# Performance work log

Measured on AMD Instinct MI355X. Metric: run time of the kernel, lower is better.

## Reference

```python
import jax, jax.numpy as jnp
import numpy as np


def setup_inputs() -> dict:
    key = jax.random.key(0)
    kq, kk, kv = jax.random.split(key, 3)
    B, H, S, D = 2, 16, 2048, 128
    q = jax.random.normal(kq, (B, H, S, D), dtype=jnp.float32)
    k = jax.random.normal(kk, (B, H, S, D), dtype=jnp.float32)
    v = jax.random.normal(kv, (B, H, S, D), dtype=jnp.float32)
    return {"q": q, "k": k, "v": v}


def reference(q, k, v):
    # qk: [B,H,S,S] full score matrix (faithful to the naive torch module)
    qk = jnp.einsum("bhsd,bhtd->bhst", q, k)
    m = jnp.max(qk, axis=-1, keepdims=True)          # row max
    p = jnp.exp(qk - m)                               # unnormalized probs
    # NOTE: original module computes lse but returns only the UNNORMALIZED o.
    o = jnp.einsum("bhst,bhtd->bhsd", p, v)
    return o
```

## Files before the change

### kernel.cpp

```cpp
#include <hip/hip_runtime.h>

typedef _Float16 f16x8  __attribute__((ext_vector_type(8)));
typedef _Float16 f16x4  __attribute__((ext_vector_type(4)));
typedef _Float16 f16x2  __attribute__((ext_vector_type(2)));
typedef float    f32x4  __attribute__((ext_vector_type(4)));
typedef float    f32x16 __attribute__((ext_vector_type(16)));
typedef int      i32x2  __attribute__((ext_vector_type(2)));

#define MFMA32(a, b, c) __builtin_amdgcn_mfma_f32_32x32x16_f16((a), (b), (c), 0, 0, 0)

static constexpr int SEQ   = 2048;
static constexpr int DIM   = 128;
static constexpr int QBLK  = 128;
static constexpr int KVBLK = 32;
static constexpr int NKT   = SEQ / KVBLK;
static constexpr int BH    = 2 * 16;
static constexpr int KSTR  = 136;
static constexpr int VSTR  = 40;

__global__ __launch_bounds__(256, 2)
void fa_fwd_kernel(const float* __restrict__ Qg, const float* __restrict__ Kg,
                   const float* __restrict__ Vg, float* __restrict__ Og)
{
    __shared__ __align__(16) _Float16 Ksh[2][KVBLK * KSTR];
    __shared__ __align__(16) _Float16 Vt[2][DIM * VSTR];

    const int tid  = threadIdx.x;
    const int wv   = tid >> 6;
    const int lane = tid & 63;
    const int lq   = lane & 31;
    const int lh   = lane >> 5;

    const int bi = blockIdx.x;
    const int bh = (bi & 7) + 8 * (bi >> 7);
    const int qt = (bi >> 3) & 15;

    const size_t base = (size_t)bh * SEQ * DIM;
    const float* Qp = Qg + base;
    const float* Kp = Kg + base;
    const float* Vp = Vg + base;
    float*       Op = Og + base;

    const int q0 = qt * QBLK + wv * 32;

    constexpr float LOG2E = 1.44269504088896340736f;
    f16x8 qh[8];
    {
        const float* qs = Qp + (size_t)(q0 + lq) * DIM + 8 * lh;
#pragma unroll
        for (int t = 0; t < 8; ++t) {
            const float4 a = *(const float4*)(qs + 16 * t);
            const float4 b = *(const float4*)(qs + 16 * t + 4);
            float xs[8] = {a.x, a.y, a.z, a.w, b.x, b.y, b.z, b.w};
            f16x8 h;
#pragma unroll
            for (int e = 0; e < 8; ++e) h[e] = (_Float16)(xs[e] * LOG2E);
            qh[t] = h;
        }
    }

    f32x16 acc[4];
#pragma unroll
    for (int a = 0; a < 4; ++a)
#pragma unroll
        for (int r = 0; r < 16; ++r) acc[a][r] = 0.0f;

    float mrow  = -3.0e38f;
    float mtrue = -3.0e38f;

    const int ksr = tid >> 3, kc0 = (tid & 7) * 16;
    const int vc  = tid & 31;
    const int vk  = (tid >> 5) * 4;
    const float* kb = Kp + (size_t)ksr * DIM + kc0;
    const float* vb = Vp + (size_t)vk * DIM + vc;

    float4 kreg[4];
    float  vreg[4][4];

    auto stage = [&](int b) {
#pragma unroll
        for (int g = 0; g < 2; ++g) {
            float xs[8] = {kreg[2*g].x, kreg[2*g].y, kreg[2*g].z, kreg[2*g].w,
                           kreg[2*g+1].x, kreg[2*g+1].y, kreg[2*g+1].z, kreg[2*g+1].w};
            f16x8 h;
#pragma unroll
            for (int e = 0; e < 8; ++e) h[e] = (_Float16)xs[e];
            *(f16x8*)((char*)&Ksh[b][0] + (ksr * KSTR + kc0 + 8 * g) * 2) = h;
        }
#pragma unroll
        for (int j = 0; j < 4; ++j) {
            const int d = vc + 32 * j;
            f16x4 tv = {(_Float16)vreg[j][0], (_Float16)vreg[j][1],
                        (_Float16)vreg[j][2], (_Float16)vreg[j][3]};
            *(f16x4*)((char*)&Vt[b][0] + (d * VSTR + vk) * 2) = tv;
        }
    };
    auto loadT = [&](int t) {
        const float* ks_ = kb + (size_t)t * KVBLK * DIM;
        const float* vs_ = vb + (size_t)t * KVBLK * DIM;
#pragma unroll
        for (int u = 0; u < 4; ++u) kreg[u] = *(const float4*)(ks_ + u * 4);
#pragma unroll
        for (int j = 0; j < 4; ++j)
#pragma unroll
            for (int r = 0; r < 4; ++r) vreg[j][r] = vs_[(size_t)r * DIM + 32 * j];
    };

    loadT(0);
    stage(0);
    loadT(1);

    for (int kt = 0; kt < NKT; ++kt) {
        const int cur = kt & 1;
        __syncthreads();

        if (kt + 1 < NKT) stage(cur ^ 1);
        if (kt + 2 < NKT) loadT(kt + 2);
        __builtin_amdgcn_sched_barrier(0);

        const char* Kc = (const char*)&Ksh[cur][0];
        const char* Vc = (const char*)&Vt[cur][0];
        f32x16 s0, s1;
#pragma unroll
        for (int r = 0; r < 16; ++r) { s0[r] = 0.0f; s1[r] = 0.0f; }
        __builtin_amdgcn_s_setprio(1);
#pragma unroll
        for (int t = 0; t < 4; ++t) {
            f16x8 ka = *(const f16x8*)(Kc + (lq * KSTR + 32 * t + 8 * lh) * 2);
            f16x8 kc = *(const f16x8*)(Kc + (lq * KSTR + 32 * t + 16 + 8 * lh) * 2);
            s0 = MFMA32(ka, qh[2 * t], s0);
            s1 = MFMA32(kc, qh[2 * t + 1], s1);
        }
        __builtin_amdgcn_s_setprio(0);
        f32x16 st = s0 + s1;

        float tmax = fmaxf(fmaxf(fmaxf(st[0], st[1]), fmaxf(st[2], st[3])),
                           fmaxf(fmaxf(st[4], st[5]), fmaxf(st[6], st[7])));
        tmax = fmaxf(tmax, fmaxf(fmaxf(fmaxf(st[8], st[9]), fmaxf(st[10], st[11])),
                                 fmaxf(fmaxf(st[12], st[13]), fmaxf(st[14], st[15]))));
        tmax = fmaxf(tmax, __shfl_xor(tmax, 32));
        mtrue = fmaxf(mtrue, tmax);

        if (!__all(tmax - mrow <= 6.0f)) {
            const float mn  = fmaxf(mrow, tmax);
            const float scl = __builtin_exp2f(mrow - mn);
            mrow = mn;
#pragma unroll
            for (int a = 0; a < 4; ++a)
#pragma unroll
                for (int r = 0; r < 16; ++r) acc[a][r] *= scl;
        }

        int pk[8];
#pragma unroll
        for (int i = 0; i < 8; ++i) {
            f16x2 e = {(_Float16)__builtin_exp2f(st[2 * i] - mrow),
                       (_Float16)__builtin_exp2f(st[2 * i + 1] - mrow)};
            pk[i] = __builtin_bit_cast(int, e);
        }

#pragma unroll
        for (int s = 0; s < 2; ++s) {
            i32x2 w02 = __builtin_amdgcn_permlane32_swap(pk[4*s+0], pk[4*s+2], false, false);
            i32x2 w13 = __builtin_amdgcn_permlane32_swap(pk[4*s+1], pk[4*s+3], false, false);
            union { int i[4]; f16x8 v; } u;
            u.i[0] = w02[0]; u.i[1] = w13[0]; u.i[2] = w02[1]; u.i[3] = w13[1];
            const f16x8 pb = u.v;
            __builtin_amdgcn_s_setprio(1);
#pragma unroll
            for (int dm = 0; dm < 4; ++dm) {
                const int d = dm * 32 + lq;
                f16x8 va = *(const f16x8*)(Vc + (d * VSTR + 16 * s + 8 * lh) * 2);
                acc[dm] = MFMA32(va, pb, acc[dm]);
            }
            __builtin_amdgcn_s_setprio(0);
        }
    }

    const float fin = __builtin_exp2f(mrow - mtrue);
#pragma unroll
    for (int a = 0; a < 4; ++a)
#pragma unroll
        for (int r = 0; r < 16; ++r) acc[a][r] *= fin;

    float* ob = Op + (size_t)(q0 + lq) * DIM + 4 * lh;
#pragma unroll
    for (int dm = 0; dm < 4; ++dm)
#pragma unroll
        for (int kp = 0; kp < 4; ++kp) {
            f32x4 v4 = {acc[dm][4*kp], acc[dm][4*kp+1], acc[dm][4*kp+2], acc[dm][4*kp+3]};
            *(f32x4*)(ob + dm * 32 + kp * 8) = v4;
        }
}

extern "C" void kernel_launch(void* const* d_in, const int* in_sizes, int n_in,
                              void* d_out, int out_size, void* d_ws, size_t ws_size,
                              hipStream_t stream) {
    const float* q = (const float*)d_in[0];
    const float* k = (const float*)d_in[1];
    const float* v = (const float*)d_in[2];
    float* o = (float*)d_out;
    dim3 grid((SEQ / QBLK) * BH);
    fa_fwd_kernel<<<grid, dim3(256), 0, stream>>>(q, k, v, o);
}
```

Before: 116.3 us.

## Double KV tile to 64 rows and speculatively compute exponentials before max update

Raises the KV tile from 32 to 64 keys, so each iteration computes two independent 32-key score blocks, halves the number of barriers, and uses wider f16x8 V-transpose stores. Exponentials are now computed with the old running max before the row max is known, and are recomputed only in the rare branch where the max grows by more than the threshold. This takes the max reduction off the critical path before the exp work. In exchange it uses more registers for the K/V prefetch and the second score block, which may hurt occupancy at 2 blocks per CU, and the LDS footprint grows.

```diff
diff --git a/kernel.cpp b/kernel.cpp
--- a/kernel.cpp
+++ b/kernel.cpp
@@ -12,11 +12,11 @@
 static constexpr int SEQ   = 2048;
 static constexpr int DIM   = 128;
 static constexpr int QBLK  = 128;
-static constexpr int KVBLK = 32;
+static constexpr int KVBLK = 64;
 static constexpr int NKT   = SEQ / KVBLK;
 static constexpr int BH    = 2 * 16;
 static constexpr int KSTR  = 136;
-static constexpr int VSTR  = 40;
+static constexpr int VSTR  = 72;
 
 __global__ __launch_bounds__(256, 2)
 void fa_fwd_kernel(const float* __restrict__ Qg, const float* __restrict__ Kg,
@@ -68,18 +68,18 @@
     float mrow  = -3.0e38f;
     float mtrue = -3.0e38f;
 
-    const int ksr = tid >> 3, kc0 = (tid & 7) * 16;
+    const int ksr = tid >> 2, kc0 = (tid & 3) * 32;
     const int vc  = tid & 31;
-    const int vk  = (tid >> 5) * 4;
+    const int vk  = (tid >> 5) * 8;
     const float* kb = Kp + (size_t)ksr * DIM + kc0;
     const float* vb = Vp + (size_t)vk * DIM + vc;
 
-    float4 kreg[4];
-    float  vreg[4][4];
+    float4 kreg[8];
+    float  vreg[4][8];
 
     auto stage = [&](int b) {
 #pragma unroll
-        for (int g = 0; g < 2; ++g) {
+        for (int g = 0; g < 4; ++g) {
             float xs[8] = {kreg[2*g].x, kreg[2*g].y, kreg[2*g].z, kreg[2*g].w,
                            kreg[2*g+1].x, kreg[2*g+1].y, kreg[2*g+1].z, kreg[2*g+1].w};
             f16x8 h;
@@ -89,21 +89,22 @@
         }
 #pragma unroll
         for (int j = 0; j < 4; ++j) {
+            f16x8 h;
+#pragma unroll
+            for (int r = 0; r < 8; ++r) h[r] = (_Float16)vreg[j][r];
             const int d = vc + 32 * j;
-            f16x4 tv = {(_Float16)vreg[j][0], (_Float16)vreg[j][1],
-                        (_Float16)vreg[j][2], (_Float16)vreg[j][3]};
-            *(f16x4*)((char*)&Vt[b][0] + (d * VSTR + vk) * 2) = tv;
+            *(f16x8*)((char*)&Vt[b][0] + (d * VSTR + vk) * 2) = h;
         }
     };
     auto loadT = [&](int t) {
         const float* ks_ = kb + (size_t)t * KVBLK * DIM;
         const float* vs_ = vb + (size_t)t * KVBLK * DIM;
 #pragma unroll
-        for (int u = 0; u < 4; ++u) kreg[u] = *(const float4*)(ks_ + u * 4);
+        for (int u = 0; u < 8; ++u) kreg[u] = *(const float4*)(ks_ + u * 4);
 #pragma unroll
         for (int j = 0; j < 4; ++j)
 #pragma unroll
-            for (int r = 0; r < 4; ++r) vreg[j][r] = vs_[(size_t)r * DIM + 32 * j];
+            for (int r = 0; r < 8; ++r) vreg[j][r] = vs_[(size_t)r * DIM + 32 * j];
     };
 
     loadT(0);
@@ -125,19 +126,28 @@
         for (int r = 0; r < 16; ++r) { s0[r] = 0.0f; s1[r] = 0.0f; }
         __builtin_amdgcn_s_setprio(1);
 #pragma unroll
-        for (int t = 0; t < 4; ++t) {
-            f16x8 ka = *(const f16x8*)(Kc + (lq * KSTR + 32 * t + 8 * lh) * 2);
-            f16x8 kc = *(const f16x8*)(Kc + (lq * KSTR + 32 * t + 16 + 8 * lh) * 2);
-            s0 = MFMA32(ka, qh[2 * t], s0);
-            s1 = MFMA32(kc, qh[2 * t + 1], s1);
+        for (int t = 0; t < 8; ++t) {
+            f16x8 ka = *(const f16x8*)(Kc + (lq * KSTR + 16 * t + 8 * lh) * 2);
+            f16x8 kc = *(const f16x8*)(Kc + ((lq + 32) * KSTR + 16 * t + 8 * lh) * 2);
+            s0 = MFMA32(ka, qh[t], s0);
+            s1 = MFMA32(kc, qh[t], s1);
         }
         __builtin_amdgcn_s_setprio(0);
-        f32x16 st = s0 + s1;
-
-        float tmax = fmaxf(fmaxf(fmaxf(st[0], st[1]), fmaxf(st[2], st[3])),
-                           fmaxf(fmaxf(st[4], st[5]), fmaxf(st[6], st[7])));
-        tmax = fmaxf(tmax, fmaxf(fmaxf(fmaxf(st[8], st[9]), fmaxf(st[10], st[11])),
-                                 fmaxf(fmaxf(st[12], st[13]), fmaxf(st[14], st[15]))));
+
+        int pk[16];
+#pragma unroll
+        for (int i = 0; i < 8; ++i) {
+            f16x2 e0 = {(_Float16)__builtin_exp2f(s0[2*i]   - mrow),
+                        (_Float16)__builtin_exp2f(s0[2*i+1] - mrow)};
+            f16x2 e1 = {(_Float16)__builtin_exp2f(s1[2*i]   - mrow),
+                        (_Float16)__builtin_exp2f(s1[2*i+1] - mrow)};
+            pk[i]     = __builtin_bit_cast(int, e0);
+            pk[8 + i] = __builtin_bit_cast(int, e1);
+        }
+
+        float tmax = fmaxf(s0[0], s1[0]);
+#pragma unroll
+        for (int r = 1; r < 16; ++r) tmax = fmaxf(tmax, fmaxf(s0[r], s1[r]));
         tmax = fmaxf(tmax, __shfl_xor(tmax, 32));
         mtrue = fmaxf(mtrue, tmax);
 
@@ -149,20 +159,23 @@
             for (int a = 0; a < 4; ++a)
 #pragma unroll
                 for (int r = 0; r < 16; ++r) acc[a][r] *= scl;
-        }
-
-        int pk[8];
-#pragma unroll
-        for (int i = 0; i < 8; ++i) {
-            f16x2 e = {(_Float16)__builtin_exp2f(st[2 * i] - mrow),
-                       (_Float16)__builtin_exp2f(st[2 * i + 1] - mrow)};
-            pk[i] = __builtin_bit_cast(int, e);
-        }
-
-#pragma unroll
-        for (int s = 0; s < 2; ++s) {
-            i32x2 w02 = __builtin_amdgcn_permlane32_swap(pk[4*s+0], pk[4*s+2], false, false);
-            i32x2 w13 = __builtin_amdgcn_permlane32_swap(pk[4*s+1], pk[4*s+3], false, false);
+#pragma unroll
+            for (int i = 0; i < 8; ++i) {
+                f16x2 e0 = {(_Float16)__builtin_exp2f(s0[2*i]   - mn),
+                            (_Float16)__builtin_exp2f(s0[2*i+1] - mn)};
+                f16x2 e1 = {(_Float16)__builtin_exp2f(s1[2*i]   - mn),
+                            (_Float16)__builtin_exp2f(s1[2*i+1] - mn)};
+                pk[i]     = __builtin_bit_cast(int, e0);
+                pk[8 + i] = __builtin_bit_cast(int, e1);
+            }
+        }
+
+#pragma unroll
+        for (int s = 0; s < 4; ++s) {
+            const int b  = (s >> 1) * 8;
+            const int sl = s & 1;
+            i32x2 w02 = __builtin_amdgcn_permlane32_swap(pk[b+4*sl+0], pk[b+4*sl+2], false, false);
+            i32x2 w13 = __builtin_amdgcn_permlane32_swap(pk[b+4*sl+1], pk[b+4*sl+3], false, false);
             union { int i[4]; f16x8 v; } u;
             u.i[0] = w02[0]; u.i[1] = w13[0]; u.i[2] = w02[1]; u.i[3] = w13[1];
             const f16x8 pb = u.v;
```

Result: slower. 125.7 us (+8.1%).

## Double-bank KV prefetch registers, use packed RTZ conversions, speculate exp before max check

Applied to the files above, without the earlier changes.

Splits the K/V prefetch registers into two banks and unrolls the main loop by two, so each global load is issued a full tile ahead and no longer waits on the previous tile's staging. This aims to overlap global latency with compute. Float-to-half conversions now use packed round-toward-zero instructions, which cuts conversion instruction count but slightly changes rounding. The exponentials are computed with the old running max before the rescale check and recomputed only when a rescale happens, which takes the max reduction off the critical path. The second register bank raises register pressure, which may hurt the two-blocks-per-CU occupancy target.

```diff
diff --git a/kernel.cpp b/kernel.cpp
--- a/kernel.cpp
+++ b/kernel.cpp
@@ -8,6 +8,7 @@
 typedef int      i32x2  __attribute__((ext_vector_type(2)));
 
 #define MFMA32(a, b, c) __builtin_amdgcn_mfma_f32_32x32x16_f16((a), (b), (c), 0, 0, 0)
+#define PKRTZ(a, b) __builtin_bit_cast(f16x2, __builtin_amdgcn_cvt_pkrtz((a), (b)))
 
 static constexpr int SEQ   = 2048;
 static constexpr int DIM   = 128;
@@ -51,11 +52,12 @@
         for (int t = 0; t < 8; ++t) {
             const float4 a = *(const float4*)(qs + 16 * t);
             const float4 b = *(const float4*)(qs + 16 * t + 4);
-            float xs[8] = {a.x, a.y, a.z, a.w, b.x, b.y, b.z, b.w};
-            f16x8 h;
-#pragma unroll
-            for (int e = 0; e < 8; ++e) h[e] = (_Float16)(xs[e] * LOG2E);
-            qh[t] = h;
+            union { f16x2 h2[4]; f16x8 v; } u;
+            u.h2[0] = PKRTZ(a.x * LOG2E, a.y * LOG2E);
+            u.h2[1] = PKRTZ(a.z * LOG2E, a.w * LOG2E);
+            u.h2[2] = PKRTZ(b.x * LOG2E, b.y * LOG2E);
+            u.h2[3] = PKRTZ(b.z * LOG2E, b.w * LOG2E);
+            qh[t] = u.v;
         }
     }
 
@@ -74,52 +76,46 @@
     const float* kb = Kp + (size_t)ksr * DIM + kc0;
     const float* vb = Vp + (size_t)vk * DIM + vc;
 
-    float4 kreg[4];
-    float  vreg[4][4];
-
-    auto stage = [&](int b) {
-#pragma unroll
-        for (int g = 0; g < 2; ++g) {
-            float xs[8] = {kreg[2*g].x, kreg[2*g].y, kreg[2*g].z, kreg[2*g].w,
-                           kreg[2*g+1].x, kreg[2*g+1].y, kreg[2*g+1].z, kreg[2*g+1].w};
-            f16x8 h;
-#pragma unroll
-            for (int e = 0; e < 8; ++e) h[e] = (_Float16)xs[e];
-            *(f16x8*)((char*)&Ksh[b][0] + (ksr * KSTR + kc0 + 8 * g) * 2) = h;
-        }
-#pragma unroll
-        for (int j = 0; j < 4; ++j) {
-            const int d = vc + 32 * j;
-            f16x4 tv = {(_Float16)vreg[j][0], (_Float16)vreg[j][1],
-                        (_Float16)vreg[j][2], (_Float16)vreg[j][3]};
-            *(f16x4*)((char*)&Vt[b][0] + (d * VSTR + vk) * 2) = tv;
-        }
-    };
-    auto loadT = [&](int t) {
-        const float* ks_ = kb + (size_t)t * KVBLK * DIM;
-        const float* vs_ = vb + (size_t)t * KVBLK * DIM;
-#pragma unroll
-        for (int u = 0; u < 4; ++u) kreg[u] = *(const float4*)(ks_ + u * 4);
-#pragma unroll
-        for (int j = 0; j < 4; ++j)
-#pragma unroll
-            for (int r = 0; r < 4; ++r) vreg[j][r] = vs_[(size_t)r * DIM + 32 * j];
-    };
-
-    loadT(0);
-    stage(0);
-    loadT(1);
-
-    for (int kt = 0; kt < NKT; ++kt) {
-        const int cur = kt & 1;
-        __syncthreads();
-
-        if (kt + 1 < NKT) stage(cur ^ 1);
-        if (kt + 2 < NKT) loadT(kt + 2);
-        __builtin_amdgcn_sched_barrier(0);
-
-        const char* Kc = (const char*)&Ksh[cur][0];
-        const char* Vc = (const char*)&Vt[cur][0];
+    float4 kregA[4], kregB[4];
+    float  vregA[4][4], vregB[4][4];
+
+#define LOAD_BANK(KR, VR, T)                                                \
+    do {                                                                    \
+        const float* ks_ = kb + (size_t)(T) * KVBLK * DIM;                  \
+        const float* vs_ = vb + (size_t)(T) * KVBLK * DIM;                  \
+        _Pragma("unroll")                                                   \
+        for (int u_ = 0; u_ < 4; ++u_) KR[u_] = *(const float4*)(ks_ + u_ * 4); \
+        _Pragma("unroll")                                                   \
+        for (int j_ = 0; j_ < 4; ++j_)                                      \
+            _Pragma("unroll")                                               \
+            for (int r_ = 0; r_ < 4; ++r_)                                  \
+                VR[j_][r_] = vs_[(size_t)r_ * DIM + 32 * j_];               \
+    } while (0)
+
+#define STAGE_BANK(KR, VR, B)                                               \
+    do {                                                                    \
+        _Pragma("unroll")                                                   \
+        for (int g_ = 0; g_ < 2; ++g_) {                                    \
+            union { f16x2 h2[4]; f16x8 v; } u_;                             \
+            u_.h2[0] = PKRTZ(KR[2*g_].x, KR[2*g_].y);                       \
+            u_.h2[1] = PKRTZ(KR[2*g_].z, KR[2*g_].w);                       \
+            u_.h2[2] = PKRTZ(KR[2*g_+1].x, KR[2*g_+1].y);                   \
+            u_.h2[3] = PKRTZ(KR[2*g_+1].z, KR[2*g_+1].w);                   \
+            *(f16x8*)((char*)&Ksh[B][0] + (ksr * KSTR + kc0 + 8 * g_) * 2) = u_.v; \
+        }                                                                   \
+        _Pragma("unroll")                                                   \
+        for (int j_ = 0; j_ < 4; ++j_) {                                    \
+            union { f16x2 h2[2]; f16x4 v; } u_;                             \
+            u_.h2[0] = PKRTZ(VR[j_][0], VR[j_][1]);                         \
+            u_.h2[1] = PKRTZ(VR[j_][2], VR[j_][3]);                         \
+            const int d_ = vc + 32 * j_;                                    \
+            *(f16x4*)((char*)&Vt[B][0] + (d_ * VSTR + vk) * 2) = u_.v;      \
+        }                                                                   \
+    } while (0)
+
+    auto computeTile = [&](int CUR) {
+        const char* Kc = (const char*)&Ksh[CUR][0];
+        const char* Vc = (const char*)&Vt[CUR][0];
         f32x16 s0, s1;
 #pragma unroll
         for (int r = 0; r < 16; ++r) { s0[r] = 0.0f; s1[r] = 0.0f; }
@@ -133,6 +129,13 @@
         }
         __builtin_amdgcn_s_setprio(0);
         f32x16 st = s0 + s1;
+
+        int pk[8];
+#pragma unroll
+        for (int i = 0; i < 8; ++i)
+            pk[i] = __builtin_bit_cast(int,
+                PKRTZ(__builtin_exp2f(st[2 * i] - mrow),
+                      __builtin_exp2f(st[2 * i + 1] - mrow)));
 
         float tmax = fmaxf(fmaxf(fmaxf(st[0], st[1]), fmaxf(st[2], st[3])),
                            fmaxf(fmaxf(st[4], st[5]), fmaxf(st[6], st[7])));
@@ -149,14 +152,11 @@
             for (int a = 0; a < 4; ++a)
 #pragma unroll
                 for (int r = 0; r < 16; ++r) acc[a][r] *= scl;
-        }
-
-        int pk[8];
-#pragma unroll
-        for (int i = 0; i < 8; ++i) {
-            f16x2 e = {(_Float16)__builtin_exp2f(st[2 * i] - mrow),
-                       (_Float16)__builtin_exp2f(st[2 * i + 1] - mrow)};
-            pk[i] = __builtin_bit_cast(int, e);
+#pragma unroll
+            for (int i = 0; i < 8; ++i)
+                pk[i] = __builtin_bit_cast(int,
+                    PKRTZ(__builtin_exp2f(st[2 * i] - mn),
+                          __builtin_exp2f(st[2 * i + 1] - mn)));
         }
 
 #pragma unroll
@@ -175,6 +175,24 @@
             }
             __builtin_amdgcn_s_setprio(0);
         }
+    };
+
+    LOAD_BANK(kregA, vregA, 0);
+    STAGE_BANK(kregA, vregA, 0);
+    LOAD_BANK(kregB, vregB, 1);
+
+    for (int kt = 0; kt < NKT; kt += 2) {
+        __syncthreads();
+        if (kt + 2 < NKT) LOAD_BANK(kregA, vregA, kt + 2);
+        __builtin_amdgcn_sched_barrier(0);
+        STAGE_BANK(kregB, vregB, 1);
+        computeTile(0);
+
+        __syncthreads();
+        if (kt + 3 < NKT) LOAD_BANK(kregB, vregB, kt + 3);
+        __builtin_amdgcn_sched_barrier(0);
+        if (kt + 2 < NKT) STAGE_BANK(kregA, vregA, 0);
+        computeTile(1);
     }
 
     const float fin = __builtin_exp2f(mrow - mtrue);
```

Result: no change. 115.4 us (-0.8%).
